# Optimization experiments

Hardware: AMD Instinct MI355X
Metric: run time of the kernel (lower is better)

Reference implementation:

```python
import jax, jax.numpy as jnp
import numpy as np

N_NODES = 50000
N_EDGES = 600000
H = 128
EPSILON = 0.7071067811865476  # layer residual scaling
EPS = 1e-08                   # norm stabilizer


def _mlp(x, W1, b1, W2, b2):
    # Linear -> silu -> Linear (blocks=2 context network)
    h = jax.nn.silu(x @ W1 + b1)
    return h @ W2 + b2


def setup_inputs() -> dict:
    key = jax.random.key(0)
    ks = jax.random.split(key, 12)
    def xav(k, fan_in, shape):
        return jax.random.normal(k, shape, jnp.float32) / jnp.sqrt(jnp.float32(fan_in))
    dir_raw = jax.random.normal(ks[2], (N_EDGES, 3), jnp.float32)
    dir_ij = dir_raw / jnp.linalg.norm(dir_raw, axis=-1, keepdims=True)
    return {
        "s": jax.random.normal(ks[0], (N_NODES, 1, H), jnp.float32),
        "v": jax.random.normal(ks[1], (N_NODES, 3, H), jnp.float32),
        "dir_ij": dir_ij,
        "Wij": jax.random.normal(ks[3], (N_EDGES, 1, 3 * H), jnp.float32),
        "senders": jax.random.randint(ks[4], (N_EDGES,), 0, N_NODES),
        "receivers": jax.random.randint(ks[5], (N_EDGES,), 0, N_NODES),
        "Wi1": xav(ks[6], H, (H, H)),
        "bi1": jnp.zeros((H,), jnp.float32),
        "Wi2": xav(ks[7], H, (H, 3 * H)),
        "bi2": jnp.zeros((3 * H,), jnp.float32),
        "Wm1": xav(ks[8], 2 * H, (2 * H, H)),
        "bm1": jnp.zeros((H,), jnp.float32),
        "Wm2": xav(ks[9], H, (H, 3 * H)),
        "bm2": jnp.zeros((3 * H,), jnp.float32),
        "Wvm": xav(ks[10], H, (H, 2 * H)),
    }


def reference(s, v, dir_ij, Wij, senders, receivers,
              Wi1, bi1, Wi2, bi2, Wm1, bm1, Wm2, bm2, Wvm):
    n_nodes = s.shape[0]
    # ---- message (inter-particle) ----
    x = _mlp(s, Wi1, bi1, Wi2, bi2)           # (N, 1, 3H)
    xj = x[receivers]                          # (E, 1, 3H) gather
    vj = v[receivers]                          # (E, 3, H)  gather
    ds_e, dv1, dv2 = jnp.split(Wij * xj, 3, axis=-1)   # each (E, 1, H)
    dv_e = dv1 * dir_ij[..., jnp.newaxis] + dv2 * vj   # (E, 3, H)
    ds = jax.ops.segment_sum(ds_e, senders, num_segments=n_nodes)
    dv = jax.ops.segment_sum(dv_e, senders, num_segments=n_nodes)
    s = (s + ds) * EPSILON
    v = (v + dv) * EPSILON
    # ---- update (intra-particle) ----
    v_l, v_r = jnp.split(v @ Wvm, 2, axis=-1)          # (N, 3, H) each
    v_norm = jnp.sqrt(jnp.sum(v_r ** 2, axis=-2, keepdims=True) + EPS)  # (N,1,H)
    ts = jnp.concatenate([s, v_norm], axis=-1)         # (N, 1, 2H)
    ds_u, dv_u, dsv = jnp.split(_mlp(ts, Wm1, bm1, Wm2, bm2), 3, axis=-1)
    dv_u = v_l * dv_u
    dsv = dsv * jnp.sum(v_r * v_l, axis=1, keepdims=True)
    s = (s + ds_u + dsv) * EPSILON                     # (N, 1, H)
    v = (v + dv_u) * EPSILON                           # (N, 3, H)
    # pack (s, v) into a single array along axis 1 -> (N, 4, H)
    return jnp.concatenate([s, v], axis=1)
```

## Files before the change

kernel.cpp:

```cpp
#include <hip/hip_runtime.h>

#define H 128
#define EPSILON 0.7071067811865476f
#define NEPS 1e-8f

typedef short bf16x8 __attribute__((ext_vector_type(8)));
typedef float f32x4 __attribute__((ext_vector_type(4)));
typedef unsigned short ushort_t;

__device__ __forceinline__ float silu_f(float x) {
    return x / (1.0f + __expf(-x));
}
__device__ __forceinline__ unsigned short bfround(float w) {
    unsigned ub = __float_as_uint(w);
    return (unsigned short)((ub + 0x7FFF + ((ub >> 16) & 1)) >> 16);
}
__device__ __forceinline__ float bfu(unsigned short u) { return __uint_as_float(((unsigned)u) << 16); }

__global__ void k_pack(const float* __restrict__ W, int K, int N,
                       ushort_t* __restrict__ p) {
    int tid = blockIdx.x * blockDim.x + threadIdx.x;
    int total = K * N;
    if (tid >= total) return;
    int CT = N >> 4;
    int j = tid & 7;
    int l = (tid >> 3) & 63;
    int rest = tid >> 9;
    int ct = rest % CT;
    int ks = rest / CT;
    int row = ks * 32 + ((l >> 4) << 3) + j;
    int col = ct * 16 + (l & 15);
    p[tid] = bfround(W[(size_t)row * N + col]);
}

__global__ void k_cvt_v(const float4* __restrict__ v4, ushort4* __restrict__ vb, int n4) {
    int i = blockIdx.x * blockDim.x + threadIdx.x;
    if (i >= n4) return;
    float4 f = v4[i];
    ushort4 u;
    u.x = bfround(f.x); u.y = bfround(f.y); u.z = bfround(f.z); u.w = bfround(f.w);
    vb[i] = u;
}

__global__ __launch_bounds__(256, 4) void k1_mfma(
        const float* __restrict__ s,
        const ushort_t* __restrict__ W1p, const ushort_t* __restrict__ W2p,
        const float* __restrict__ bi1, const float* __restrict__ bi2,
        ushort_t* __restrict__ x, int n_nodes) {
    __shared__ ushort_t Ab[16 * 136];
    __shared__ ushort_t Hb[16 * 136];
    int t = threadIdx.x;
    int node0 = blockIdx.x * 16;
    int wv = t >> 6, lane = t & 63;
    int g = lane >> 4, cl = lane & 15;

    #pragma unroll
    for (int i = 0; i < 8; ++i) {
        int flat = t + i * 256;
        int n = flat >> 7, k = flat & 127;
        int node = node0 + n; if (node >= n_nodes) node = n_nodes - 1;
        Ab[n * 136 + k] = bfround(s[(size_t)node * 128 + k]);
    }
    __syncthreads();

    f32x4 acc1[2] = {};
    #pragma unroll
    for (int ks = 0; ks < 4; ++ks) {
        bf16x8 ah = *(const bf16x8*)&Ab[cl * 136 + ks * 32 + g * 8];
        #pragma unroll
        for (int c = 0; c < 2; ++c) {
            int ct = wv * 2 + c;
            bf16x8 bh = *(const bf16x8*)&W1p[((size_t)(ks * 8 + ct) * 64 + lane) * 8];
            acc1[c] = __builtin_amdgcn_mfma_f32_16x16x32_bf16(ah, bh, acc1[c], 0, 0, 0);
        }
    }
    #pragma unroll
    for (int c = 0; c < 2; ++c) {
        int col = (wv * 2 + c) * 16 + cl;
        float bias = bi1[col];
        #pragma unroll
        for (int r = 0; r < 4; ++r) {
            int row = g * 4 + r;
            Hb[row * 136 + col] = bfround(silu_f(acc1[c][r] + bias));
        }
    }
    __syncthreads();

    f32x4 acc2[6] = {};
    #pragma unroll
    for (int ks = 0; ks < 4; ++ks) {
        bf16x8 ah = *(const bf16x8*)&Hb[cl * 136 + ks * 32 + g * 8];
        #pragma unroll
        for (int c = 0; c < 6; ++c) {
            int ct = wv * 6 + c;
            bf16x8 bh = *(const bf16x8*)&W2p[((size_t)(ks * 24 + ct) * 64 + lane) * 8];
            acc2[c] = __builtin_amdgcn_mfma_f32_16x16x32_bf16(ah, bh, acc2[c], 0, 0, 0);
        }
    }
    #pragma unroll
    for (int c = 0; c < 6; ++c) {
        int col = (wv * 6 + c) * 16 + cl;
        float bias = bi2[col];
        #pragma unroll
        for (int r = 0; r < 4; ++r) {
            int node = node0 + g * 4 + r;
            if (node < n_nodes) x[(size_t)node * 384 + col] = bfround(acc2[c][r] + bias);
        }
    }
}

__global__ void k_hist(const int* __restrict__ senders, int* __restrict__ cnt, int n_edges) {
    int e = blockIdx.x * blockDim.x + threadIdx.x;
    if (e < n_edges) atomicAdd(&cnt[senders[e]], 1);
}

__global__ void k_alloc(const int* __restrict__ cnt, int* __restrict__ starts,
                        int* __restrict__ head, int* __restrict__ cursor, int n) {
    int i = blockIdx.x * blockDim.x + threadIdx.x;
    int lane = threadIdx.x & 63;
    int c = (i < n) ? cnt[i] : 0;
    int pref = c;
    #pragma unroll
    for (int off = 1; off < 64; off <<= 1) {
        int up = __shfl_up(pref, off, 64);
        if (lane >= off) pref += up;
    }
    int total = __shfl(pref, 63, 64);
    int base = 0;
    if (lane == 63) base = atomicAdd(cursor, total);
    base = __shfl(base, 63, 64);
    if (i < n) { int p = base + pref - c; starts[i] = p; head[i] = p; }
}

__global__ void k_scatter(const int* __restrict__ senders, const int* __restrict__ receivers,
                          int* __restrict__ head, int* __restrict__ eord,
                          int* __restrict__ erecv, int n_edges) {
    int e = blockIdx.x * blockDim.x + threadIdx.x;
    if (e < n_edges) {
        int p = atomicAdd(&head[senders[e]], 1);
        eord[p] = e;
        erecv[p] = receivers[e];
    }
}

__global__ __launch_bounds__(256) void k2_csr(
        const float4* __restrict__ s4, const ushort_t* __restrict__ vbf,
        const ushort_t* __restrict__ xbf, const float* __restrict__ dir,
        const float4* __restrict__ w4, const int* __restrict__ starts,
        const int* __restrict__ cnt, const int* __restrict__ eord,
        const int* __restrict__ erecv, float4* __restrict__ out4, int n_nodes) {
    __shared__ float4 red[8][128];
    int node = blockIdx.x;
    int t = threadIdx.x;
    int slot = t >> 5, lane = t & 31;
    int beg = starts[node], num = cnt[node];
    float4 ds  = {0.f, 0.f, 0.f, 0.f};
    float4 dv0 = {0.f, 0.f, 0.f, 0.f};
    float4 dv1 = {0.f, 0.f, 0.f, 0.f};
    float4 dv2 = {0.f, 0.f, 0.f, 0.f};
    for (int q = slot; q < num; q += 8) {
        int e = eord[beg + q];
        int r = erecv[beg + q];
        const float4*   we = w4  + (size_t)e * 96;
        const ushort_t* xr = xbf + (size_t)r * 384;
        const ushort_t* vr = vbf + (size_t)r * 384;
        float4 wa = we[lane], wb = we[32 + lane], wc = we[64 + lane];
        ushort4 xa = *(const ushort4*)&xr[4 * lane];
        ushort4 xb = *(const ushort4*)&xr[128 + 4 * lane];
        ushort4 xc = *(const ushort4*)&xr[256 + 4 * lane];
        ushort4 va = *(const ushort4*)&vr[4 * lane];
        ushort4 vb = *(const ushort4*)&vr[128 + 4 * lane];
        ushort4 vc = *(const ushort4*)&vr[256 + 4 * lane];
        float d0 = dir[3 * (size_t)e + 0];
        float d1 = dir[3 * (size_t)e + 1];
        float d2 = dir[3 * (size_t)e + 2];
        float bx = wb.x * bfu(xb.x), by = wb.y * bfu(xb.y), bz = wb.z * bfu(xb.z), bw = wb.w * bfu(xb.w);
        float cx = wc.x * bfu(xc.x), cy = wc.y * bfu(xc.y), cz = wc.z * bfu(xc.z), cw = wc.w * bfu(xc.w);
        ds.x += wa.x * bfu(xa.x); ds.y += wa.y * bfu(xa.y);
        ds.z += wa.z * bfu(xa.z); ds.w += wa.w * bfu(xa.w);
        dv0.x += bx * d0 + cx * bfu(va.x); dv0.y += by * d0 + cy * bfu(va.y);
        dv0.z += bz * d0 + cz * bfu(va.z); dv0.w += bw * d0 + cw * bfu(va.w);
        dv1.x += bx * d1 + cx * bfu(vb.x); dv1.y += by * d1 + cy * bfu(vb.y);
        dv1.z += bz * d1 + cz * bfu(vb.z); dv1.w += bw * d1 + cw * bfu(vb.w);
        dv2.x += bx * d2 + cx * bfu(vc.x); dv2.y += by * d2 + cy * bfu(vc.y);
        dv2.z += bz * d2 + cz * bfu(vc.z); dv2.w += bw * d2 + cw * bfu(vc.w);
    }
    red[slot][lane]      = ds;
    red[slot][32 + lane] = dv0;
    red[slot][64 + lane] = dv1;
    red[slot][96 + lane] = dv2;
    __syncthreads();
    if (t < 128) {
        float4 acc = red[0][t];
        #pragma unroll
        for (int q2 = 1; q2 < 8; ++q2) {
            float4 r2 = red[q2][t];
            acc.x += r2.x; acc.y += r2.y; acc.z += r2.z; acc.w += r2.w;
        }
        int which = t >> 5, hh = t & 31;
        float4 base;
        if (which == 0) base = s4[(size_t)node * 32 + hh];
        else {
            base = ((const float4*)0)[0];
        }
        if (which != 0) {
            const float4* vrow = (const float4*)((const char*)s4 + 0);
        }
        float4 o;
        o.x = (base.x + acc.x) * EPSILON;
        o.y = (base.y + acc.y) * EPSILON;
        o.z = (base.z + acc.z) * EPSILON;
        o.w = (base.w + acc.w) * EPSILON;
        out4[(size_t)node * 128 + t] = o;
    }
}

__global__ __launch_bounds__(256) void k2_csr2(
        const float4* __restrict__ s4, const float4* __restrict__ v4,
        const ushort_t* __restrict__ vbf, const ushort_t* __restrict__ xbf,
        const float* __restrict__ dir, const float4* __restrict__ w4,
        const int* __restrict__ starts, const int* __restrict__ cnt,
        const int* __restrict__ eord, const int* __restrict__ erecv,
        float4* __restrict__ out4, int n_nodes) {
    __shared__ float4 red[8][128];
    int node = blockIdx.x;
    int t = threadIdx.x;
    int slot = t >> 5, lane = t & 31;
    int beg = starts[node], num = cnt[node];
    float4 ds  = {0.f, 0.f, 0.f, 0.f};
    float4 dv0 = {0.f, 0.f, 0.f, 0.f};
    float4 dv1 = {0.f, 0.f, 0.f, 0.f};
    float4 dv2 = {0.f, 0.f, 0.f, 0.f};
    for (int q = slot; q < num; q += 8) {
        int e = eord[beg + q];
        int r = erecv[beg + q];
        const float4*   we = w4  + (size_t)e * 96;
        const ushort_t* xr = xbf + (size_t)r * 384;
        const ushort_t* vr = vbf + (size_t)r * 384;
        float4 wa = we[lane], wb = we[32 + lane], wc = we[64 + lane];
        ushort4 xa = *(const ushort4*)&xr[4 * lane];
        ushort4 xb = *(const ushort4*)&xr[128 + 4 * lane];
        ushort4 xc = *(const ushort4*)&xr[256 + 4 * lane];
        ushort4 va = *(const ushort4*)&vr[4 * lane];
        ushort4 vb = *(const ushort4*)&vr[128 + 4 * lane];
        ushort4 vc = *(const ushort4*)&vr[256 + 4 * lane];
        float d0 = dir[3 * (size_t)e + 0];
        float d1 = dir[3 * (size_t)e + 1];
        float d2 = dir[3 * (size_t)e + 2];
        float bx = wb.x * bfu(xb.x), by = wb.y * bfu(xb.y), bz = wb.z * bfu(xb.z), bw = wb.w * bfu(xb.w);
        float cx = wc.x * bfu(xc.x), cy = wc.y * bfu(xc.y), cz = wc.z * bfu(xc.z), cw = wc.w * bfu(xc.w);
        ds.x += wa.x * bfu(xa.x); ds.y += wa.y * bfu(xa.y);
        ds.z += wa.z * bfu(xa.z); ds.w += wa.w * bfu(xa.w);
        dv0.x += bx * d0 + cx * bfu(va.x); dv0.y += by * d0 + cy * bfu(va.y);
        dv0.z += bz * d0 + cz * bfu(va.z); dv0.w += bw * d0 + cw * bfu(va.w);
        dv1.x += bx * d1 + cx * bfu(vb.x); dv1.y += by * d1 + cy * bfu(vb.y);
        dv1.z += bz * d1 + cz * bfu(vb.z); dv1.w += bw * d1 + cw * bfu(vb.w);
        dv2.x += bx * d2 + cx * bfu(vc.x); dv2.y += by * d2 + cy * bfu(vc.y);
        dv2.z += bz * d2 + cz * bfu(vc.z); dv2.w += bw * d2 + cw * bfu(vc.w);
    }
    red[slot][lane]      = ds;
    red[slot][32 + lane] = dv0;
    red[slot][64 + lane] = dv1;
    red[slot][96 + lane] = dv2;
    __syncthreads();
    if (t < 128) {
        float4 acc = red[0][t];
        #pragma unroll
        for (int q2 = 1; q2 < 8; ++q2) {
            float4 r2 = red[q2][t];
            acc.x += r2.x; acc.y += r2.y; acc.z += r2.z; acc.w += r2.w;
        }
        int which = t >> 5, hh = t & 31;
        float4 base;
        if (which == 0) base = s4[(size_t)node * 32 + hh];
        else            base = v4[(size_t)node * 96 + (size_t)(which - 1) * 32 + hh];
        float4 o;
        o.x = (base.x + acc.x) * EPSILON;
        o.y = (base.y + acc.y) * EPSILON;
        o.z = (base.z + acc.z) * EPSILON;
        o.w = (base.w + acc.w) * EPSILON;
        out4[(size_t)node * 128 + t] = o;
    }
}

__global__ __launch_bounds__(256, 2) void k3_mfma(
        const ushort_t* __restrict__ Wvp, const ushort_t* __restrict__ W1p,
        const ushort_t* __restrict__ W2p,
        const float* __restrict__ bm1, const float* __restrict__ bm2,
        float* __restrict__ out, int n_nodes) {
    __shared__ __align__(16) char pool[51968];
    ushort_t* Ab  = (ushort_t*)pool;
    ushort_t* vlb = (ushort_t*)(pool + 13056);
    ushort_t* vrc = (ushort_t*)(pool + 26112);
    ushort_t* Tb  = (ushort_t*)(pool + 39168);
    ushort_t* Hb  = (ushort_t*)(pool + 47616);
    float* C3 = (float*)(pool + 26112);

    int t = threadIdx.x;
    int node0 = blockIdx.x * 16;
    int wv = t >> 6, lane = t & 63;
    int g = lane >> 4, cl = lane & 15;

    float smid_reg[8], dot_reg[8];

    #pragma unroll
    for (int i = 0; i < 24; ++i) {
        int flat = t + i * 256;
        int row = flat >> 7, k = flat & 127;
        int n = row / 3, d = row - n * 3;
        int node = node0 + n; if (node >= n_nodes) node = n_nodes - 1;
        Ab[row * 136 + k] = bfround(out[(size_t)node * 512 + 128 + d * 128 + k]);
    }
    #pragma unroll
    for (int i = 0; i < 8; ++i) {
        int flat = t + i * 256;
        int n = flat >> 7, k = flat & 127;
        int node = node0 + n; if (node >= n_nodes) node = n_nodes - 1;
        smid_reg[i] = out[(size_t)node * 512 + k];
    }
    __syncthreads();

    #pragma unroll
    for (int rt = 0; rt < 3; ++rt) {
        bf16x8 ah[4];
        #pragma unroll
        for (int ks = 0; ks < 4; ++ks)
            ah[ks] = *(const bf16x8*)&Ab[(rt * 16 + cl) * 136 + ks * 32 + g * 8];
        f32x4 acc[4] = {};
        #pragma unroll
        for (int ks = 0; ks < 4; ++ks) {
            #pragma unroll
            for (int c = 0; c < 4; ++c) {
                int ct = wv * 4 + c;
                bf16x8 bh = *(const bf16x8*)&Wvp[((size_t)(ks * 16 + ct) * 64 + lane) * 8];
                acc[c] = __builtin_amdgcn_mfma_f32_16x16x32_bf16(ah[ks], bh, acc[c], 0, 0, 0);
            }
        }
        #pragma unroll
        for (int c = 0; c < 4; ++c) {
            int col = (wv * 4 + c) * 16 + cl;
            ushort_t* dst = (col < 128) ? vlb : vrc;
            int cc = col & 127;
            #pragma unroll
            for (int r = 0; r < 4; ++r)
                dst[(rt * 16 + g * 4 + r) * 136 + cc] = bfround(acc[c][r]);
        }
    }
    __syncthreads();

    #pragma unroll
    for (int i = 0; i < 8; ++i) {
        int flat = t + i * 256;
        int n = flat >> 7, h = flat & 127;
        float r0 = bfu(vrc[(3 * n + 0) * 136 + h]);
        float r1 = bfu(vrc[(3 * n + 1) * 136 + h]);
        float r2 = bfu(vrc[(3 * n + 2) * 136 + h]);
        float l0 = bfu(vlb[(3 * n + 0) * 136 + h]);
        float l1 = bfu(vlb[(3 * n + 1) * 136 + h]);
        float l2 = bfu(vlb[(3 * n + 2) * 136 + h]);
        float nrm = sqrtf(r0 * r0 + r1 * r1 + r2 * r2 + NEPS);
        dot_reg[i] = r0 * l0 + r1 * l1 + r2 * l2;
        Tb[n * 264 + 128 + h] = bfround(nrm);
        Tb[n * 264 + h] = bfround(smid_reg[i]);
    }
    __syncthreads();

    f32x4 acc2[2] = {};
    #pragma unroll
    for (int ks = 0; ks < 8; ++ks) {
        bf16x8 ah = *(const bf16x8*)&Tb[cl * 264 + ks * 32 + g * 8];
        #pragma unroll
        for (int c = 0; c < 2; ++c) {
            int ct = wv * 2 + c;
            bf16x8 bh = *(const bf16x8*)&W1p[((size_t)(ks * 8 + ct) * 64 + lane) * 8];
            acc2[c] = __builtin_amdgcn_mfma_f32_16x16x32_bf16(ah, bh, acc2[c], 0, 0, 0);
        }
    }
    #pragma unroll
    for (int c = 0; c < 2; ++c) {
        int col = (wv * 2 + c) * 16 + cl;
        float bias = bm1[col];
        #pragma unroll
        for (int r = 0; r < 4; ++r) {
            int row = g * 4 + r;
            Hb[row * 136 + col] = bfround(silu_f(acc2[c][r] + bias));
        }
    }
    __syncthreads();

    f32x4 acc3[6] = {};
    #pragma unroll
    for (int ks = 0; ks < 4; ++ks) {
        bf16x8 ah = *(const bf16x8*)&Hb[cl * 136 + ks * 32 + g * 8];
        #pragma unroll
        for (int c = 0; c < 6; ++c) {
            int ct = wv * 6 + c;
            bf16x8 bh = *(const bf16x8*)&W2p[((size_t)(ks * 24 + ct) * 64 + lane) * 8];
            acc3[c] = __builtin_amdgcn_mfma_f32_16x16x32_bf16(ah, bh, acc3[c], 0, 0, 0);
        }
    }
    __syncthreads();
    #pragma unroll
    for (int c = 0; c < 6; ++c) {
        int col = (wv * 6 + c) * 16 + cl;
        float bias = bm2[col];
        #pragma unroll
        for (int r = 0; r < 4; ++r)
            C3[(g * 4 + r) * 400 + col] = acc3[c][r] + bias;
    }
    __syncthreads();

    #pragma unroll
    for (int i = 0; i < 8; ++i) {
        int flat = t + i * 256;
        int n = flat >> 7, h = flat & 127;
        int node = node0 + n;
        if (node >= n_nodes) continue;
        float ds_u = C3[n * 400 + h];
        float dv_u = C3[n * 400 + 128 + h];
        float dsv  = C3[n * 400 + 256 + h] * dot_reg[i];
        out[(size_t)node * 512 + h] = (smid_reg[i] + ds_u + dsv) * EPSILON;
        #pragma unroll
        for (int d = 0; d < 3; ++d) {
            int row = 3 * n + d;
            float vmid = bfu(Ab[row * 136 + h]);
            float vl_v = bfu(vlb[row * 136 + h]);
            out[(size_t)node * 512 + 128 + d * 128 + h] = (vmid + vl_v * dv_u) * EPSILON;
        }
    }
}

static inline size_t align_up(size_t x, size_t a) { return (x + a - 1) / a * a; }

extern "C" void kernel_launch(void* const* d_in, const int* in_sizes, int n_in,
                              void* d_out, int out_size, void* d_ws, size_t ws_size,
                              hipStream_t stream) {
    const float* s       = (const float*)d_in[0];
    const float* v       = (const float*)d_in[1];
    const float* dir     = (const float*)d_in[2];
    const float* Wij     = (const float*)d_in[3];
    const int*   senders = (const int*)d_in[4];
    const int*   recv    = (const int*)d_in[5];
    const float* Wi1     = (const float*)d_in[6];
    const float* bi1     = (const float*)d_in[7];
    const float* Wi2     = (const float*)d_in[8];
    const float* bi2     = (const float*)d_in[9];
    const float* Wm1     = (const float*)d_in[10];
    const float* bm1     = (const float*)d_in[11];
    const float* Wm2     = (const float*)d_in[12];
    const float* bm2     = (const float*)d_in[13];
    const float* Wvm     = (const float*)d_in[14];

    int n_nodes = in_sizes[0] / H;
    int n_edges = in_sizes[4];
    float* out = (float*)d_out;

    char* ws = (char*)d_ws;
    size_t off = 0;
    ushort_t* x   = (ushort_t*)(ws + off); off = align_up(off + (size_t)n_nodes * 384 * 2, 256);
    ushort_t* vbf = (ushort_t*)(ws + off); off = align_up(off + (size_t)n_nodes * 384 * 2, 256);
    int* starts = (int*)(ws + off); off = align_up(off + (size_t)n_nodes * 4, 256);
    int* cnt    = (int*)(ws + off); off = align_up(off + (size_t)(n_nodes + 1) * 4, 256);
    int* cursor = cnt + n_nodes;
    int* head   = (int*)(ws + off); off = align_up(off + (size_t)n_nodes * 4, 256);
    int* eord   = (int*)(ws + off); off = align_up(off + (size_t)n_edges * 4, 256);
    int* erecv  = (int*)(ws + off); off = align_up(off + (size_t)n_edges * 4, 256);
    ushort_t* Wi1p = (ushort_t*)(ws + off); off = align_up(off + 16384 * 2, 256);
    ushort_t* Wi2p = (ushort_t*)(ws + off); off = align_up(off + 49152 * 2, 256);
    ushort_t* Wvp  = (ushort_t*)(ws + off); off = align_up(off + 32768 * 2, 256);
    ushort_t* Wm1p = (ushort_t*)(ws + off); off = align_up(off + 32768 * 2, 256);
    ushort_t* Wm2p = (ushort_t*)(ws + off); off = align_up(off + 49152 * 2, 256);
    if (off > ws_size) return;

    hipMemsetAsync(cnt, 0, (size_t)(n_nodes + 1) * 4, stream);
    k_hist<<<(n_edges + 255) / 256, 256, 0, stream>>>(senders, cnt, n_edges);
    k_alloc<<<(n_nodes + 255) / 256, 256, 0, stream>>>(cnt, starts, head, cursor, n_nodes);
    k_scatter<<<(n_edges + 255) / 256, 256, 0, stream>>>(senders, recv, head, eord, erecv, n_edges);

    k_pack<<<(128 * 128 + 255) / 256, 256, 0, stream>>>(Wi1, 128, 128, Wi1p);
    k_pack<<<(128 * 384 + 255) / 256, 256, 0, stream>>>(Wi2, 128, 384, Wi2p);
    k_pack<<<(128 * 256 + 255) / 256, 256, 0, stream>>>(Wvm, 128, 256, Wvp);
    k_pack<<<(256 * 128 + 255) / 256, 256, 0, stream>>>(Wm1, 256, 128, Wm1p);
    k_pack<<<(128 * 384 + 255) / 256, 256, 0, stream>>>(Wm2, 128, 384, Wm2p);
    int n4 = n_nodes * 96;
    k_cvt_v<<<(n4 + 255) / 256, 256, 0, stream>>>((const float4*)v, (ushort4*)vbf, n4);

    k1_mfma<<<(n_nodes + 15) / 16, 256, 0, stream>>>(
        s, Wi1p, Wi2p, bi1, bi2, x, n_nodes);

    k2_csr2<<<n_nodes, 256, 0, stream>>>(
        (const float4*)s, (const float4*)v, vbf, x, dir,
        (const float4*)Wij, starts, cnt, eord, erecv, (float4*)out, n_nodes);

    k3_mfma<<<(n_nodes + 15) / 16, 256, 0, stream>>>(
        Wvp, Wm1p, Wm2p, bm1, bm2, out, n_nodes);
}
```

Before: 527.4 us.

## Merge prep kernels and pass bf16 intermediate between aggregation and update

Combines the counter memset, five weight-pack launches and the v conversion into one grid-stride prep kernel, cutting launch count. The edge aggregation kernel now writes its intermediate (s,v) as bf16 to a separate workspace buffer instead of fp32 into the output, and takes the v residual base from the bf16 copy. The update kernel then reads the bf16 intermediate directly with vector loads, halving intermediate traffic. The cost is extra rounding: the v residual and intermediate s are stored in bf16, which lowers accuracy.

```diff
diff --git a/kernel.cpp b/kernel.cpp
--- a/kernel.cpp
+++ b/kernel.cpp
@@ -17,11 +17,8 @@
 }
 __device__ __forceinline__ float bfu(unsigned short u) { return __uint_as_float(((unsigned)u) << 16); }
 
-__global__ void k_pack(const float* __restrict__ W, int K, int N,
-                       ushort_t* __restrict__ p) {
-    int tid = blockIdx.x * blockDim.x + threadIdx.x;
-    int total = K * N;
-    if (tid >= total) return;
+__device__ __forceinline__ void pack_one(const float* __restrict__ W, int N,
+                                         ushort_t* __restrict__ p, int tid) {
     int CT = N >> 4;
     int j = tid & 7;
     int l = (tid >> 3) & 63;
@@ -33,13 +30,38 @@
     p[tid] = bfround(W[(size_t)row * N + col]);
 }
 
-__global__ void k_cvt_v(const float4* __restrict__ v4, ushort4* __restrict__ vb, int n4) {
-    int i = blockIdx.x * blockDim.x + threadIdx.x;
-    if (i >= n4) return;
-    float4 f = v4[i];
-    ushort4 u;
-    u.x = bfround(f.x); u.y = bfround(f.y); u.z = bfround(f.z); u.w = bfround(f.w);
-    vb[i] = u;
+__global__ void k_prep(const float* __restrict__ Wi1, const float* __restrict__ Wi2,
+                       const float* __restrict__ Wvm, const float* __restrict__ Wm1,
+                       const float* __restrict__ Wm2,
+                       ushort_t* __restrict__ Wi1p, ushort_t* __restrict__ Wi2p,
+                       ushort_t* __restrict__ Wvp, ushort_t* __restrict__ Wm1p,
+                       ushort_t* __restrict__ Wm2p,
+                       const float4* __restrict__ v4, ushort4* __restrict__ vb,
+                       int* __restrict__ cnt, int n_cnt, int n4) {
+    int gid = blockIdx.x * blockDim.x + threadIdx.x;
+    int stride = gridDim.x * blockDim.x;
+    int S0 = n_cnt;
+    int S1 = S0 + 16384;
+    int S2 = S1 + 49152;
+    int S3 = S2 + 32768;
+    int S4 = S3 + 32768;
+    int S5 = S4 + 49152;
+    int S6 = S5 + n4;
+    for (int i = gid; i < S6; i += stride) {
+        if (i < S0)      cnt[i] = 0;
+        else if (i < S1) pack_one(Wi1, 128, Wi1p, i - S0);
+        else if (i < S2) pack_one(Wi2, 384, Wi2p, i - S1);
+        else if (i < S3) pack_one(Wvm, 256, Wvp,  i - S2);
+        else if (i < S4) pack_one(Wm1, 128, Wm1p, i - S3);
+        else if (i < S5) pack_one(Wm2, 384, Wm2p, i - S4);
+        else {
+            int j = i - S5;
+            float4 f = v4[j];
+            ushort4 u;
+            u.x = bfround(f.x); u.y = bfround(f.y); u.z = bfround(f.z); u.w = bfround(f.w);
+            vb[j] = u;
+        }
+    }
 }
 
 __global__ __launch_bounds__(256, 4) void k1_mfma(
@@ -143,12 +165,12 @@
     }
 }
 
-__global__ __launch_bounds__(256) void k2_csr(
+__global__ __launch_bounds__(256) void k2_csr3(
         const float4* __restrict__ s4, const ushort_t* __restrict__ vbf,
         const ushort_t* __restrict__ xbf, const float* __restrict__ dir,
         const float4* __restrict__ w4, const int* __restrict__ starts,
         const int* __restrict__ cnt, const int* __restrict__ eord,
-        const int* __restrict__ erecv, float4* __restrict__ out4, int n_nodes) {
+        const int* __restrict__ erecv, ushort_t* __restrict__ mid, int n_nodes) {
     __shared__ float4 red[8][128];
     int node = blockIdx.x;
     int t = threadIdx.x;
@@ -199,91 +221,23 @@
         }
         int which = t >> 5, hh = t & 31;
         float4 base;
-        if (which == 0) base = s4[(size_t)node * 32 + hh];
-        else {
-            base = ((const float4*)0)[0];
-        }
-        if (which != 0) {
-            const float4* vrow = (const float4*)((const char*)s4 + 0);
-        }
-        float4 o;
-        o.x = (base.x + acc.x) * EPSILON;
-        o.y = (base.y + acc.y) * EPSILON;
-        o.z = (base.z + acc.z) * EPSILON;
-        o.w = (base.w + acc.w) * EPSILON;
-        out4[(size_t)node * 128 + t] = o;
-    }
-}
-
-__global__ __launch_bounds__(256) void k2_csr2(
-        const float4* __restrict__ s4, const float4* __restrict__ v4,
-        const ushort_t* __restrict__ vbf, const ushort_t* __restrict__ xbf,
-        const float* __restrict__ dir, const float4* __restrict__ w4,
-        const int* __restrict__ starts, const int* __restrict__ cnt,
-        const int* __restrict__ eord, const int* __restrict__ erecv,
-        float4* __restrict__ out4, int n_nodes) {
-    __shared__ float4 red[8][128];
-    int node = blockIdx.x;
-    int t = threadIdx.x;
-    int slot = t >> 5, lane = t & 31;
-    int beg = starts[node], num = cnt[node];
-    float4 ds  = {0.f, 0.f, 0.f, 0.f};
-    float4 dv0 = {0.f, 0.f, 0.f, 0.f};
-    float4 dv1 = {0.f, 0.f, 0.f, 0.f};
-    float4 dv2 = {0.f, 0.f, 0.f, 0.f};
-    for (int q = slot; q < num; q += 8) {
-        int e = eord[beg + q];
-        int r = erecv[beg + q];
-        const float4*   we = w4  + (size_t)e * 96;
-        const ushort_t* xr = xbf + (size_t)r * 384;
-        const ushort_t* vr = vbf + (size_t)r * 384;
-        float4 wa = we[lane], wb = we[32 + lane], wc = we[64 + lane];
-        ushort4 xa = *(const ushort4*)&xr[4 * lane];
-        ushort4 xb = *(const ushort4*)&xr[128 + 4 * lane];
-        ushort4 xc = *(const ushort4*)&xr[256 + 4 * lane];
-        ushort4 va = *(const ushort4*)&vr[4 * lane];
-        ushort4 vb = *(const ushort4*)&vr[128 + 4 * lane];
-        ushort4 vc = *(const ushort4*)&vr[256 + 4 * lane];
-        float d0 = dir[3 * (size_t)e + 0];
-        float d1 = dir[3 * (size_t)e + 1];
-        float d2 = dir[3 * (size_t)e + 2];
-        float bx = wb.x * bfu(xb.x), by = wb.y * bfu(xb.y), bz = wb.z * bfu(xb.z), bw = wb.w * bfu(xb.w);
-        float cx = wc.x * bfu(xc.x), cy = wc.y * bfu(xc.y), cz = wc.z * bfu(xc.z), cw = wc.w * bfu(xc.w);
-        ds.x += wa.x * bfu(xa.x); ds.y += wa.y * bfu(xa.y);
-        ds.z += wa.z * bfu(xa.z); ds.w += wa.w * bfu(xa.w);
-        dv0.x += bx * d0 + cx * bfu(va.x); dv0.y += by * d0 + cy * bfu(va.y);
-        dv0.z += bz * d0 + cz * bfu(va.z); dv0.w += bw * d0 + cw * bfu(va.w);
-        dv1.x += bx * d1 + cx * bfu(vb.x); dv1.y += by * d1 + cy * bfu(vb.y);
-        dv1.z += bz * d1 + cz * bfu(vb.z); dv1.w += bw * d1 + cw * bfu(vb.w);
-        dv2.x += bx * d2 + cx * bfu(vc.x); dv2.y += by * d2 + cy * bfu(vc.y);
-        dv2.z += bz * d2 + cz * bfu(vc.z); dv2.w += bw * d2 + cw * bfu(vc.w);
-    }
-    red[slot][lane]      = ds;
-    red[slot][32 + lane] = dv0;
-    red[slot][64 + lane] = dv1;
-    red[slot][96 + lane] = dv2;
-    __syncthreads();
-    if (t < 128) {
-        float4 acc = red[0][t];
-        #pragma unroll
-        for (int q2 = 1; q2 < 8; ++q2) {
-            float4 r2 = red[q2][t];
-            acc.x += r2.x; acc.y += r2.y; acc.z += r2.z; acc.w += r2.w;
-        }
-        int which = t >> 5, hh = t & 31;
-        float4 base;
-        if (which == 0) base = s4[(size_t)node * 32 + hh];
-        else            base = v4[(size_t)node * 96 + (size_t)(which - 1) * 32 + hh];
-        float4 o;
-        o.x = (base.x + acc.x) * EPSILON;
-        o.y = (base.y + acc.y) * EPSILON;
-        o.z = (base.z + acc.z) * EPSILON;
-        o.w = (base.w + acc.w) * EPSILON;
-        out4[(size_t)node * 128 + t] = o;
+        if (which == 0) {
+            base = s4[(size_t)node * 32 + hh];
+        } else {
+            ushort4 u = *(const ushort4*)&vbf[(size_t)node * 384 + (size_t)(which - 1) * 128 + 4 * hh];
+            base.x = bfu(u.x); base.y = bfu(u.y); base.z = bfu(u.z); base.w = bfu(u.w);
+        }
+        ushort4 o;
+        o.x = bfround((base.x + acc.x) * EPSILON);
+        o.y = bfround((base.y + acc.y) * EPSILON);
+        o.z = bfround((base.z + acc.z) * EPSILON);
+        o.w = bfround((base.w + acc.w) * EPSILON);
+        *(ushort4*)&mid[(size_t)node * 512 + 4 * t] = o;
     }
 }
 
 __global__ __launch_bounds__(256, 2) void k3_mfma(
+        const ushort_t* __restrict__ mid,
         const ushort_t* __restrict__ Wvp, const ushort_t* __restrict__ W1p,
         const ushort_t* __restrict__ W2p,
         const float* __restrict__ bm1, const float* __restrict__ bm2,
@@ -304,19 +258,20 @@
     float smid_reg[8], dot_reg[8];
 
     #pragma unroll
-    for (int i = 0; i < 24; ++i) {
-        int flat = t + i * 256;
-        int row = flat >> 7, k = flat & 127;
+    for (int i = 0; i < 6; ++i) {
+        int flat4 = t + i * 256;
+        int row = flat4 >> 5, k4 = flat4 & 31;
         int n = row / 3, d = row - n * 3;
         int node = node0 + n; if (node >= n_nodes) node = n_nodes - 1;
-        Ab[row * 136 + k] = bfround(out[(size_t)node * 512 + 128 + d * 128 + k]);
+        ushort4 u = *(const ushort4*)&mid[(size_t)node * 512 + (size_t)(1 + d) * 128 + 4 * k4];
+        *(ushort4*)&Ab[row * 136 + 4 * k4] = u;
     }
     #pragma unroll
     for (int i = 0; i < 8; ++i) {
         int flat = t + i * 256;
         int n = flat >> 7, k = flat & 127;
         int node = node0 + n; if (node >= n_nodes) node = n_nodes - 1;
-        smid_reg[i] = out[(size_t)node * 512 + k];
+        smid_reg[i] = bfu(mid[(size_t)node * 512 + k]);
     }
     __syncthreads();
 
@@ -459,6 +414,7 @@
     size_t off = 0;
     ushort_t* x   = (ushort_t*)(ws + off); off = align_up(off + (size_t)n_nodes * 384 * 2, 256);
     ushort_t* vbf = (ushort_t*)(ws + off); off = align_up(off + (size_t)n_nodes * 384 * 2, 256);
+    ushort_t* mid = (ushort_t*)(ws + off); off = align_up(off + (size_t)n_nodes * 512 * 2, 256);
     int* starts = (int*)(ws + off); off = align_up(off + (size_t)n_nodes * 4, 256);
     int* cnt    = (int*)(ws + off); off = align_up(off + (size_t)(n_nodes + 1) * 4, 256);
     int* cursor = cnt + n_nodes;
@@ -472,26 +428,25 @@
     ushort_t* Wm2p = (ushort_t*)(ws + off); off = align_up(off + 49152 * 2, 256);
     if (off > ws_size) return;
 
-    hipMemsetAsync(cnt, 0, (size_t)(n_nodes + 1) * 4, stream);
+    int n4 = n_nodes * 96;
+    int prep_total = (n_nodes + 1) + 16384 + 49152 + 32768 + 32768 + 49152 + n4;
+    int prep_blocks = (prep_total + 255) / 256;
+    if (prep_blocks > 2048) prep_blocks = 2048;
+    k_prep<<<prep_blocks, 256, 0, stream>>>(
+        Wi1, Wi2, Wvm, Wm1, Wm2, Wi1p, Wi2p, Wvp, Wm1p, Wm2p,
+        (const float4*)v, (ushort4*)vbf, cnt, n_nodes + 1, n4);
+
     k_hist<<<(n_edges + 255) / 256, 256, 0, stream>>>(senders, cnt, n_edges);
     k_alloc<<<(n_nodes + 255) / 256, 256, 0, stream>>>(cnt, starts, head, cursor, n_nodes);
     k_scatter<<<(n_edges + 255) / 256, 256, 0, stream>>>(senders, recv, head, eord, erecv, n_edges);
 
-    k_pack<<<(128 * 128 + 255) / 256, 256, 0, stream>>>(Wi1, 128, 128, Wi1p);
-    k_pack<<<(128 * 384 + 255) / 256, 256, 0, stream>>>(Wi2, 128, 384, Wi2p);
-    k_pack<<<(128 * 256 + 255) / 256, 256, 0, stream>>>(Wvm, 128, 256, Wvp);
-    k_pack<<<(256 * 128 + 255) / 256, 256, 0, stream>>>(Wm1, 256, 128, Wm1p);
-    k_pack<<<(128 * 384 + 255) / 256, 256, 0, stream>>>(Wm2, 128, 384, Wm2p);
-    int n4 = n_nodes * 96;
-    k_cvt_v<<<(n4 + 255) / 256, 256, 0, stream>>>((const float4*)v, (ushort4*)vbf, n4);
-
     k1_mfma<<<(n_nodes + 15) / 16, 256, 0, stream>>>(
         s, Wi1p, Wi2p, bi1, bi2, x, n_nodes);
 
-    k2_csr2<<<n_nodes, 256, 0, stream>>>(
-        (const float4*)s, (const float4*)v, vbf, x, dir,
-        (const float4*)Wij, starts, cnt, eord, erecv, (float4*)out, n_nodes);
+    k2_csr3<<<n_nodes, 256, 0, stream>>>(
+        (const float4*)s, vbf, x, dir,
+        (const float4*)Wij, starts, cnt, eord, erecv, mid, n_nodes);
 
     k3_mfma<<<(n_nodes + 15) / 16, 256, 0, stream>>>(
-        Wvp, Wm1p, Wm2p, bm1, bm2, out, n_nodes);
-}
+        mid, Wvp, Wm1p, Wm2p, bm1, bm2, out, n_nodes);
+}
```

Measured after the change: 483.2 us. 1.09x faster.
